# Performance work log

Measured on AMD Instinct MI355X. Metric: run time of the kernel, lower is better.

## Reference

```python
import jax, jax.numpy as jnp
import numpy as np

E1, E2, A = 400000, 100000, 400000
F1, F2, FA, H = 128, 128, 8, 128


def _linear_init(key, fan_in, fan_out):
    # torch nn.Linear default: U(-1/sqrt(fan_in), 1/sqrt(fan_in)) for W and b
    kw, kb = jax.random.split(key)
    bound = 1.0 / np.sqrt(fan_in)
    W = jax.random.uniform(kw, (fan_in, fan_out), jnp.float32, -bound, bound)
    b = jax.random.uniform(kb, (fan_out,), jnp.float32, -bound, bound)
    return W, b


def setup_inputs() -> dict:
    key = jax.random.key(0)
    ks = jax.random.split(key, 10)
    e1 = jax.random.normal(ks[0], (E1, F1), jnp.float32)
    e2 = jax.random.normal(ks[1], (E2, F2), jnp.float32)
    a12 = jax.random.normal(ks[2], (A, FA), jnp.float32)
    row = jax.random.randint(ks[3], (A,), 0, E1)
    col = jax.random.randint(ks[4], (A,), 0, E2)
    angle_index12 = jnp.stack([row, col], axis=0)
    aW0, ab0 = _linear_init(ks[5], FA + F1 + F2, H)
    aW1, ab1 = _linear_init(ks[6], H, H)
    aW2, ab2 = _linear_init(ks[7], H, H)
    eW0, eb0 = _linear_init(ks[8], H + F2, H)
    k9a, k9b = jax.random.split(ks[9])
    eW1, eb1 = _linear_init(k9a, H, H)
    eW2, eb2 = _linear_init(k9b, H, H)
    return {"e1": e1, "e2": e2, "a12": a12, "angle_index12": angle_index12,
            "aW0": aW0, "ab0": ab0, "aW1": aW1, "ab1": ab1, "aW2": aW2, "ab2": ab2,
            "eW0": eW0, "eb0": eb0, "eW1": eW1, "eb1": eb1, "eW2": eW2, "eb2": eb2}


def _mlp(x, W0, b0, W1, b1, W2, b2):
    # linear -> SELU -> linear -> SELU -> linear (no final activation)
    h = jax.nn.selu(x @ W0 + b0)
    h = jax.nn.selu(h @ W1 + b1)
    return h @ W2 + b2


def reference(e1, e2, a12, angle_index12,
              aW0, ab0, aW1, ab1, aW2, ab2,
              eW0, eb0, eW1, eb1, eW2, eb2):
    row, col = angle_index12[0], angle_index12[1]
    # gather + concat: [A, FA+F1+F2]
    x = jnp.concatenate([a12, e1[row], e2[col]], axis=1)
    a = _mlp(x, aW0, ab0, aW1, ab1, aW2, ab2)  # [A, H]
    n2 = e2.shape[0]
    sums = jax.ops.segment_sum(a, col, num_segments=n2)  # [E2, H]
    cnt = jax.ops.segment_sum(jnp.ones((a.shape[0], 1), a.dtype), col, num_segments=n2)
    aggr = sums / jnp.maximum(cnt, 1.0)  # scatter-mean
    return _mlp(jnp.concatenate([aggr, e2], axis=1), eW0, eb0, eW1, eb1, eW2, eb2)
```

## Files before the change

### kernel.cpp

```cpp
#include <hip/hip_runtime.h>
#include <hip/hip_bf16.h>


using u16    = unsigned short;
using u16x8  = __attribute__((ext_vector_type(8))) unsigned short;
using bf16x8 = __attribute__((ext_vector_type(8))) short;
using f32x4  = __attribute__((ext_vector_type(4))) float;

constexpr int H   = 128;
constexpr int NTH = 256;

__device__ __forceinline__ u16 f2bf(float f) {
    union { float f; unsigned u; } x; x.f = f;
    unsigned r = x.u + 0x7FFFu + ((x.u >> 16) & 1u);
    return (u16)(r >> 16);
}
__device__ __forceinline__ unsigned cvt2(float x, float y) {
    union { __hip_bfloat162 h; unsigned u; } c;
    c.h = __float22bfloat162_rn(make_float2(x, y));
    return c.u;
}
__device__ __forceinline__ bf16x8 cvt8(float4 a, float4 b) {
    union { unsigned u[4]; bf16x8 v; } o;
    o.u[0] = cvt2(a.x, a.y); o.u[1] = cvt2(a.z, a.w);
    o.u[2] = cvt2(b.x, b.y); o.u[3] = cvt2(b.z, b.w);
    return o.v;
}
__device__ __forceinline__ float4 ld4(const float* p) { return *(const float4*)p; }
__device__ __forceinline__ float selu_f(float x) {
    const float scale = 1.0507009873554804934193349852946f;
    const float sa    = 1.0507009873554805f * 1.6732632423543772848170429916717f;
    return x > 0.0f ? scale * x : sa * (__expf(x) - 1.0f);
}

__device__ __forceinline__ void load_wchunk(const u16* __restrict__ wt, int KPu, int c,
                                            int tid, u16x8 st[4]) {
#pragma unroll
    for (int s = 0; s < 4; ++s) {
        int i = s * NTH + tid;
        int n = i >> 3, jj = i & 7;
        st[s] = *(const u16x8*)(wt + (size_t)n * KPu + (c * 8 + jj) * 8);
    }
}
__device__ __forceinline__ void write_wchunk(u16* wb, int tid, const u16x8 st[4]) {
#pragma unroll
    for (int s = 0; s < 4; ++s) {
        int i = s * NTH + tid;
        *(u16x8*)(wb + i * 8) = st[s];
    }
}

template<int NKS>
__device__ __forceinline__ void mfma_chunk(const u16* cur, const bf16x8* afc,
                                           int ml, int kq, f32x4 acc[8]) {
#pragma unroll
    for (int ks = 0; ks < NKS; ++ks) {
        bf16x8 a = afc[ks];
#pragma unroll
        for (int sc = 0; sc < 8; ++sc) {
            bf16x8 b = *(const bf16x8*)&cur[(sc * 16 + ml) * 64 +
                                            (((ks * 4 + kq) ^ (ml & 7)) << 3)];
            acc[sc] = __builtin_amdgcn_mfma_f32_16x16x32_bf16(a, b, acc[sc], 0, 0, 0);
        }
    }
}

template<int NCHUNK, int LAST_NKS>
__device__ __forceinline__ void stream_layer(const u16* __restrict__ wt, int KPu,
                                             const bf16x8* af, u16* wb0, u16* wb1,
                                             int tid, int ml, int kq, f32x4 acc[8]) {
    u16x8 st[4];
    load_wchunk(wt, KPu, 0, tid, st);
    write_wchunk(wb0, tid, st);
    __syncthreads();
#pragma unroll
    for (int c = 0; c < NCHUNK; ++c) {
        u16* cur = (c & 1) ? wb1 : wb0;
        u16* nxt = (c & 1) ? wb0 : wb1;
        if (c + 1 < NCHUNK) load_wchunk(wt, KPu, c + 1, tid, st);
        if (c == NCHUNK - 1) mfma_chunk<LAST_NKS>(cur, af + 2 * c, ml, kq, acc);
        else                 mfma_chunk<2>(cur, af + 2 * c, ml, kq, acc);
        if (c + 1 < NCHUNK) write_wchunk(nxt, tid, st);
        __syncthreads();
    }
}

__device__ __forceinline__ void preload2_layer(const u16* __restrict__ wt,
                                               const bf16x8* af, u16* wb0, u16* wb1,
                                               int tid, int ml, int kq, f32x4 acc[8]) {
    u16x8 s0[4], s1[4];
    load_wchunk(wt, 128, 0, tid, s0);
    load_wchunk(wt, 128, 1, tid, s1);
    write_wchunk(wb0, tid, s0);
    write_wchunk(wb1, tid, s1);
    __syncthreads();
    mfma_chunk<2>(wb0, af + 0, ml, kq, acc);
    mfma_chunk<2>(wb1, af + 2, ml, kq, acc);
}

__device__ __forceinline__ void init_acc(const float* __restrict__ b, int ml, f32x4 acc[8]) {
#pragma unroll
    for (int sc = 0; sc < 8; ++sc) {
        float bv = b[sc * 16 + ml];
        acc[sc] = f32x4{bv, bv, bv, bv};
    }
}

__device__ __forceinline__ void store_h_selu(const f32x4 acc[8], u16* hbuf,
                                             int w, int ml, int kq) {
#pragma unroll
    for (int sc = 0; sc < 8; ++sc)
#pragma unroll
        for (int r = 0; r < 4; r += 2) {
            unsigned u = cvt2(selu_f(acc[sc][r]), selu_f(acc[sc][r + 1]));
            int rowb = w * 16 + kq * 4 + r;
            hbuf[rowb * 136 + sc * 16 + ml]       = (u16)u;
            hbuf[(rowb + 1) * 136 + sc * 16 + ml] = (u16)(u >> 16);
        }
}
__device__ __forceinline__ void read_af_h(const u16* hbuf, int w, int ml, int kq,
                                          bf16x8 af[4]) {
#pragma unroll
    for (int f = 0; f < 4; ++f)
        af[f] = *(const bf16x8*)&hbuf[(w * 16 + ml) * 136 + f * 32 + kq * 8];
}

__global__ void prep_weights(const float* __restrict__ aW0, const float* __restrict__ aW1,
                             const float* __restrict__ aW2, const float* __restrict__ eW0,
                             const float* __restrict__ eW1, const float* __restrict__ eW2,
                             u16* __restrict__ dst)
{
    int t = blockIdx.x * 256 + threadIdx.x;
    const int nbs[6]  = {40, 16, 16, 32, 16, 16};
    const int Ks[6]   = {264, 128, 128, 256, 128, 128};
    const int offs[6] = {0, 40960, 57344, 73728, 106496, 122880};
    const float* Ws[6] = {aW0, aW1, aW2, eW0, eW1, eW2};
    int m = 0, rem = t;
    for (m = 0; m < 6; ++m) { int c = 128 * nbs[m]; if (rem < c) break; rem -= c; }
    if (m >= 6) return;
    const int nb = nbs[m];
    const int n = rem / nb, j = rem % nb;
    const int c = j >> 3, jj = j & 7;
    const int kb = jj ^ (n & 7);
    const int k0 = c * 64 + kb * 8;
    const int K = Ks[m];
    const float* W = Ws[m];
    union { u16 u[8]; u16x8 v; } o;
#pragma unroll
    for (int i = 0; i < 8; ++i) {
        int k = k0 + i;
        o.u[i] = (k < K) ? f2bf(W[k * H + n]) : (u16)0;
    }
    *(u16x8*)&dst[offs[m] + n * (nb * 8) + j * 8] = o.v;
}

__global__ __launch_bounds__(NTH, 3) void angle_mlp(
    const float* __restrict__ e1, const float* __restrict__ e2,
    const float* __restrict__ a12, const int* __restrict__ idx,
    const u16* __restrict__ wt0, const u16* __restrict__ wt1, const u16* __restrict__ wt2,
    const float* __restrict__ b0, const float* __restrict__ b1, const float* __restrict__ b2,
    float* __restrict__ sums, float* __restrict__ cnt, int A)
{
    __shared__ u16 wbuf[2][128 * 64];
    __shared__ u16 hbuf[64 * 136];

    const int tid = threadIdx.x;
    const int lane = tid & 63;
    const int ml = lane & 15, kq = lane >> 4;
    const int w = tid >> 6;
    const int ebase = blockIdx.x * 64;
    const int e = ebase + w * 16 + ml;
    const int rw = idx[e];
    const int cl = idx[A + e];
    if (kq == 0) atomicAdd(&cnt[cl], 1.0f);

    bf16x8 af[9];
    {
        const float* p1 = e1 + (size_t)rw * H;
        const float* p2 = e2 + (size_t)cl * H;
#pragma unroll
        for (int f = 0; f < 8; ++f) {
            int k0 = f * 32 + kq * 8;
            const float* p = (k0 == 0) ? (a12 + (size_t)e * 8)
                           : (k0 <= 128 ? p1 + (k0 - 8) : p2 + (k0 - 136));
            af[f] = cvt8(ld4(p), ld4(p + 4));
        }
        if (kq == 0) af[8] = cvt8(ld4(p2 + 120), ld4(p2 + 124));
        else { bf16x8 z = {0,0,0,0,0,0,0,0}; af[8] = z; }
    }

    f32x4 acc[8];
    init_acc(b0, ml, acc);
    stream_layer<5, 1>(wt0, 320, af, wbuf[0], wbuf[1], tid, ml, kq, acc);

    store_h_selu(acc, hbuf, w, ml, kq);
    __syncthreads();
    bf16x8 af1[4];
    read_af_h(hbuf, w, ml, kq, af1);
    init_acc(b1, ml, acc);
    preload2_layer(wt1, af1, wbuf[0], wbuf[1], tid, ml, kq, acc);

    __syncthreads();
    store_h_selu(acc, hbuf, w, ml, kq);
    __syncthreads();
    bf16x8 af2[4];
    read_af_h(hbuf, w, ml, kq, af2);
    init_acc(b2, ml, acc);
    preload2_layer(wt2, af2, wbuf[0], wbuf[1], tid, ml, kq, acc);

#pragma unroll
    for (int r = 0; r < 4; ++r) {
        int clr = idx[A + ebase + w * 16 + kq * 4 + r];
        float* dst = sums + (size_t)clr * H + ml;
#pragma unroll
        for (int sc = 0; sc < 8; ++sc)
            atomicAdd(dst + sc * 16, acc[sc][r]);
    }
}

__global__ __launch_bounds__(NTH, 3) void edge_mlp(
    const float* __restrict__ e2, const float* __restrict__ sums,
    const float* __restrict__ cnt,
    const u16* __restrict__ wt0, const u16* __restrict__ wt1, const u16* __restrict__ wt2,
    const float* __restrict__ b0, const float* __restrict__ b1, const float* __restrict__ b2,
    float* __restrict__ out, int E2n)
{
    __shared__ u16 wbuf[2][128 * 64];
    __shared__ u16 hbuf[64 * 136];

    const int tid = threadIdx.x;
    const int lane = tid & 63;
    const int ml = lane & 15, kq = lane >> 4;
    const int w = tid >> 6;
    const int nbase = blockIdx.x * 64;
    const int node = nbase + w * 16 + ml;
    const int nc = node < E2n ? node : E2n - 1;

    const float rcp = 1.0f / fmaxf(cnt[nc], 1.0f);
    bf16x8 af[8];
    {
        const float* ps = sums + (size_t)nc * H;
        const float* p2 = e2 + (size_t)nc * H;
#pragma unroll
        for (int f = 0; f < 8; ++f) {
            int k0 = f * 32 + kq * 8;
            bool agg = k0 < 128;
            const float* p = agg ? ps + k0 : p2 + (k0 - 128);
            float4 lo = ld4(p), hi = ld4(p + 4);
            float s = agg ? rcp : 1.0f;
            lo.x *= s; lo.y *= s; lo.z *= s; lo.w *= s;
            hi.x *= s; hi.y *= s; hi.z *= s; hi.w *= s;
            af[f] = cvt8(lo, hi);
        }
    }

    f32x4 acc[8];
    init_acc(b0, ml, acc);
    stream_layer<4, 2>(wt0, 256, af, wbuf[0], wbuf[1], tid, ml, kq, acc);

    store_h_selu(acc, hbuf, w, ml, kq);
    __syncthreads();
    bf16x8 af1[4];
    read_af_h(hbuf, w, ml, kq, af1);
    init_acc(b1, ml, acc);
    preload2_layer(wt1, af1, wbuf[0], wbuf[1], tid, ml, kq, acc);

    __syncthreads();
    store_h_selu(acc, hbuf, w, ml, kq);
    __syncthreads();
    bf16x8 af2[4];
    read_af_h(hbuf, w, ml, kq, af2);
    init_acc(b2, ml, acc);
    preload2_layer(wt2, af2, wbuf[0], wbuf[1], tid, ml, kq, acc);

#pragma unroll
    for (int r = 0; r < 4; ++r) {
        int nrow = nbase + w * 16 + kq * 4 + r;
        if (nrow < E2n) {
            float* dst = out + (size_t)nrow * H + ml;
#pragma unroll
            for (int sc = 0; sc < 8; ++sc)
                dst[sc * 16] = acc[sc][r];
        }
    }
}

extern "C" void kernel_launch(void* const* d_in, const int* in_sizes, int n_in,
                              void* d_out, int out_size, void* d_ws, size_t ws_size,
                              hipStream_t stream)
{
    const float* e1  = (const float*)d_in[0];
    const float* e2  = (const float*)d_in[1];
    const float* a12 = (const float*)d_in[2];
    const int*   idx = (const int*)d_in[3];
    const float* aW0 = (const float*)d_in[4];
    const float* ab0 = (const float*)d_in[5];
    const float* aW1 = (const float*)d_in[6];
    const float* ab1 = (const float*)d_in[7];
    const float* aW2 = (const float*)d_in[8];
    const float* ab2 = (const float*)d_in[9];
    const float* eW0 = (const float*)d_in[10];
    const float* eb0 = (const float*)d_in[11];
    const float* eW1 = (const float*)d_in[12];
    const float* eb1 = (const float*)d_in[13];
    const float* eW2 = (const float*)d_in[14];
    const float* eb2 = (const float*)d_in[15];

    const int E2n = in_sizes[1] / H;
    const int A   = in_sizes[2] / 8;

    char* ws = (char*)d_ws;
    u16*   wdst = (u16*)ws;
    float* sums = (float*)(ws + 278528);
    float* cnt  = sums + (size_t)E2n * H;

    hipMemsetAsync(sums, 0, ((size_t)E2n * H + E2n) * sizeof(float), stream);
    prep_weights<<<dim3(68), dim3(256), 0, stream>>>(aW0, aW1, aW2, eW0, eW1, eW2, wdst);

    angle_mlp<<<dim3(A / 64), dim3(NTH), 0, stream>>>(
        e1, e2, a12, idx, wdst + 0, wdst + 40960, wdst + 57344,
        ab0, ab1, ab2, sums, cnt, A);

    edge_mlp<<<dim3((E2n + 63) / 64), dim3(NTH), 0, stream>>>(
        e2, sums, cnt, wdst + 73728, wdst + 106496, wdst + 122880,
        eb0, eb1, eb2, (float*)d_out, E2n);
}
```

Before: 305.5 us.

## Accumulate scatter sums in fp16 with packed atomic adds

The segment-sum buffer switches from fp32 to fp16. The angle kernel pairs neighbouring lanes with shuffles so each lane issues a packed two-element fp16 atomic add, which halves the atomic count and the memory traffic of the scatter. The edge kernel reads the fp16 sums and converts them back to float before the mean. This risks precision loss in the accumulated sums, since about four values per node are summed in fp16, and it also shrinks the memset.

```diff
diff --git a/kernel.cpp b/kernel.cpp
--- a/kernel.cpp
+++ b/kernel.cpp
@@ -1,5 +1,6 @@
 #include <hip/hip_runtime.h>
 #include <hip/hip_bf16.h>
+#include <hip/hip_fp16.h>
 
 
 using u16    = unsigned short;
@@ -27,6 +28,10 @@
     return o.v;
 }
 __device__ __forceinline__ float4 ld4(const float* p) { return *(const float4*)p; }
+__device__ __forceinline__ float h2f(u16 u) {
+    union { u16 u; __half h; } c; c.u = u;
+    return __half2float(c.h);
+}
 __device__ __forceinline__ float selu_f(float x) {
     const float scale = 1.0507009873554804934193349852946f;
     const float sa    = 1.0507009873554805f * 1.6732632423543772848170429916717f;
@@ -159,7 +164,7 @@
     const float* __restrict__ a12, const int* __restrict__ idx,
     const u16* __restrict__ wt0, const u16* __restrict__ wt1, const u16* __restrict__ wt2,
     const float* __restrict__ b0, const float* __restrict__ b1, const float* __restrict__ b2,
-    float* __restrict__ sums, float* __restrict__ cnt, int A)
+    u16* __restrict__ sums, float* __restrict__ cnt, int A)
 {
     __shared__ u16 wbuf[2][128 * 64];
     __shared__ u16 hbuf[64 * 136];
@@ -208,18 +213,33 @@
     init_acc(b2, ml, acc);
     preload2_layer(wt2, af2, wbuf[0], wbuf[1], tid, ml, kq, acc);
 
-#pragma unroll
-    for (int r = 0; r < 4; ++r) {
-        int clr = idx[A + ebase + w * 16 + kq * 4 + r];
-        float* dst = sums + (size_t)clr * H + ml;
-#pragma unroll
-        for (int sc = 0; sc < 8; ++sc)
-            atomicAdd(dst + sc * 16, acc[sc][r]);
+    const int rb = (ml & 1) * 2;
+    const int i0 = A + ebase + w * 16 + kq * 4;
+    const int clr0 = idx[i0 + rb];
+    const int clr1 = idx[i0 + rb + 1];
+#pragma unroll
+    for (int sc = 0; sc < 8; ++sc) {
+        float p0 = __shfl_xor(acc[sc][0], 1);
+        float p1 = __shfl_xor(acc[sc][1], 1);
+        float p2 = __shfl_xor(acc[sc][2], 1);
+        float p3 = __shfl_xor(acc[sc][3], 1);
+        float o0 = acc[sc][rb], o1 = acc[sc][rb + 1];
+        float q0 = (ml & 1) ? p2 : p0;
+        float q1 = (ml & 1) ? p3 : p1;
+        float l0 = (ml & 1) ? q0 : o0, h0 = (ml & 1) ? o0 : q0;
+        float l1 = (ml & 1) ? q1 : o1, h1 = (ml & 1) ? o1 : q1;
+        union { __half2 h; unsigned u; } c0, c1;
+        c0.h = __floats2half2_rn(l0, h0);
+        c1.h = __floats2half2_rn(l1, h1);
+        u16* d0 = sums + (size_t)clr0 * H + sc * 16 + (ml & ~1);
+        u16* d1 = sums + (size_t)clr1 * H + sc * 16 + (ml & ~1);
+        asm volatile("global_atomic_pk_add_f16 %0, %1, off" :: "v"(d0), "v"(c0.u) : "memory");
+        asm volatile("global_atomic_pk_add_f16 %0, %1, off" :: "v"(d1), "v"(c1.u) : "memory");
     }
 }
 
 __global__ __launch_bounds__(NTH, 3) void edge_mlp(
-    const float* __restrict__ e2, const float* __restrict__ sums,
+    const float* __restrict__ e2, const u16* __restrict__ sums,
     const float* __restrict__ cnt,
     const u16* __restrict__ wt0, const u16* __restrict__ wt1, const u16* __restrict__ wt2,
     const float* __restrict__ b0, const float* __restrict__ b1, const float* __restrict__ b2,
@@ -239,17 +259,22 @@
     const float rcp = 1.0f / fmaxf(cnt[nc], 1.0f);
     bf16x8 af[8];
     {
-        const float* ps = sums + (size_t)nc * H;
+        const u16* ps = sums + (size_t)nc * H;
         const float* p2 = e2 + (size_t)nc * H;
 #pragma unroll
         for (int f = 0; f < 8; ++f) {
             int k0 = f * 32 + kq * 8;
-            bool agg = k0 < 128;
-            const float* p = agg ? ps + k0 : p2 + (k0 - 128);
-            float4 lo = ld4(p), hi = ld4(p + 4);
-            float s = agg ? rcp : 1.0f;
-            lo.x *= s; lo.y *= s; lo.z *= s; lo.w *= s;
-            hi.x *= s; hi.y *= s; hi.z *= s; hi.w *= s;
+            float4 lo, hi;
+            if (k0 < 128) {
+                u16x8 hv = *(const u16x8*)(ps + k0);
+                lo.x = h2f(hv[0]) * rcp; lo.y = h2f(hv[1]) * rcp;
+                lo.z = h2f(hv[2]) * rcp; lo.w = h2f(hv[3]) * rcp;
+                hi.x = h2f(hv[4]) * rcp; hi.y = h2f(hv[5]) * rcp;
+                hi.z = h2f(hv[6]) * rcp; hi.w = h2f(hv[7]) * rcp;
+            } else {
+                lo = ld4(p2 + (k0 - 128));
+                hi = ld4(p2 + (k0 - 124));
+            }
             af[f] = cvt8(lo, hi);
         }
     }
@@ -310,18 +335,18 @@
     const int A   = in_sizes[2] / 8;
 
     char* ws = (char*)d_ws;
-    u16*   wdst = (u16*)ws;
-    float* sums = (float*)(ws + 278528);
-    float* cnt  = sums + (size_t)E2n * H;
-
-    hipMemsetAsync(sums, 0, ((size_t)E2n * H + E2n) * sizeof(float), stream);
+    u16*   wdst   = (u16*)ws;
+    u16*   sums_h = (u16*)(ws + 278528);
+    float* cnt    = (float*)(ws + 278528 + (size_t)E2n * H * 2);
+
+    hipMemsetAsync(sums_h, 0, (size_t)E2n * H * 2 + (size_t)E2n * 4, stream);
     prep_weights<<<dim3(68), dim3(256), 0, stream>>>(aW0, aW1, aW2, eW0, eW1, eW2, wdst);
 
     angle_mlp<<<dim3(A / 64), dim3(NTH), 0, stream>>>(
         e1, e2, a12, idx, wdst + 0, wdst + 40960, wdst + 57344,
-        ab0, ab1, ab2, sums, cnt, A);
+        ab0, ab1, ab2, sums_h, cnt, A);
 
     edge_mlp<<<dim3((E2n + 63) / 64), dim3(NTH), 0, stream>>>(
-        e2, sums, cnt, wdst + 73728, wdst + 106496, wdst + 122880,
+        e2, sums_h, cnt, wdst + 73728, wdst + 106496, wdst + 122880,
         eb0, eb1, eb2, (float*)d_out, E2n);
 }
```

Measured after the change: 295.7 us. 3.2% less time.
